# Performance work log

Hardware: AMD Instinct MI355X
Metric: run time of the kernel (lower is better)

Reference implementation:

```python
import jax, jax.numpy as jnp
import numpy as np

DIM = 1536
NHEADS = 24
HEAD_DIM = DIM // NHEADS
EPS = 1e-6


def rms_norm(x):
    # normalize over last dim, no learned weight
    ms = jnp.mean(x * x, axis=-1, keepdims=True)
    return x * jax.lax.rsqrt(ms + EPS)


def rope_non_neox(x, cos, sin):
    # x: [B, S, H, D]; cos/sin: [S, D] -> broadcast [1, S, 1, D]
    # non-neox (GPT-J / interleaved) style: pairs are (x0,x1),(x2,x3),...
    c = cos[None, :, None, :]
    s = sin[None, :, None, :]
    x1 = x[..., 0::2]
    x2 = x[..., 1::2]
    c1 = c[..., 0::2]
    s1 = s[..., 0::2]
    o1 = x1 * c1 - x2 * s1
    o2 = x2 * c1 + x1 * s1
    out = jnp.stack([o1, o2], axis=-1).reshape(x.shape)
    return out


def setup_inputs() -> dict:
    key = jax.random.key(0)
    k1, k2, k3, k4, k5 = jax.random.split(key, 5)
    B, S = 4, 4096
    x = jax.random.normal(k1, (B, S, DIM), dtype=jnp.float32)
    # rotary tables: build valid cos/sin from random angles (interleaved duplication)
    half = HEAD_DIM // 2
    inv_freq = 1.0 / (10000.0 ** (jnp.arange(0, half, dtype=jnp.float32) / half))
    t = jnp.arange(S, dtype=jnp.float32)
    freqs = jnp.outer(t, inv_freq)  # [S, D/2]
    cos = jnp.repeat(jnp.cos(freqs), 2, axis=-1)  # [S, D] interleaved
    sin = jnp.repeat(jnp.sin(freqs), 2, axis=-1)
    w_qkv = jax.random.normal(k2, (DIM, 3 * DIM), dtype=jnp.float32) * (DIM ** -0.5)
    b_qkv = jax.random.normal(k3, (3 * DIM,), dtype=jnp.float32) * 0.02
    return {"x": x, "cos": cos, "sin": sin, "w_qkv": w_qkv, "b_qkv": b_qkv}


def reference(x, cos, sin, w_qkv, b_qkv):
    B, S, _ = x.shape
    H, D = NHEADS, HEAD_DIM
    qkv = jnp.einsum('bsd,de->bse', x, w_qkv) + b_qkv  # [B,S,3*DIM]
    q, k, v = jnp.split(qkv, 3, axis=-1)
    q = q.reshape(B, S, H, D)
    k = k.reshape(B, S, H, D)
    v = v.reshape(B, S, H, D)
    q = rms_norm(q)
    k = rms_norm(k)
    q = rope_non_neox(q, cos, sin)
    k = rope_non_neox(k, cos, sin)
    # SDPA: [B,H,S,D]
    qh = q.transpose(0, 2, 1, 3)
    kh = k.transpose(0, 2, 1, 3)
    vh = v.transpose(0, 2, 1, 3)
    scale = D ** -0.5
    scores = jnp.einsum('bhqd,bhkd->bhqk', qh, kh) * scale
    attn = jax.nn.softmax(scores, axis=-1)
    out = jnp.einsum('bhqk,bhkd->bhqd', attn, vh)
    out = out.transpose(0, 2, 1, 3).reshape(B, S, H * D)
    return out
```

## Files before the change

### kernel.cpp

```cpp
#include <hip/hip_runtime.h>

#define DIM   1536
#define NQKV  4608
#define NH    24
#define HD    64
#define BATCH 4
#define SEQ   4096
#define ROWS  16384

typedef _Float16 f16x8 __attribute__((ext_vector_type(8)));
typedef float    f32x4 __attribute__((ext_vector_type(4)));

__device__ __forceinline__ void gload_lds16(const void* g, void* l) {
  __builtin_amdgcn_global_load_lds(
      (const __attribute__((address_space(1))) unsigned int*)g,
      (__attribute__((address_space(3))) unsigned int*)l, 16, 0, 0);
}
__device__ __forceinline__ float fexp2(float x) {
#if __has_builtin(__builtin_amdgcn_exp2f)
  return __builtin_amdgcn_exp2f(x);
#else
  return exp2f(x);
#endif
}

#define QSCALE 0.18033688011112042f

__global__ __launch_bounds__(256) void convert_x(const float* __restrict__ X,
                                                 _Float16* __restrict__ Xh) {
  const int i = (blockIdx.x * 256 + threadIdx.x) * 8;
  float4 a = *(const float4*)(X + i);
  float4 b = *(const float4*)(X + i + 4);
  f16x8 h;
  h[0] = (_Float16)a.x; h[1] = (_Float16)a.y; h[2] = (_Float16)a.z; h[3] = (_Float16)a.w;
  h[4] = (_Float16)b.x; h[5] = (_Float16)b.y; h[6] = (_Float16)b.z; h[7] = (_Float16)b.w;
  *(f16x8*)(Xh + i) = h;
}

__global__ __launch_bounds__(256) void transpose_w(const float* __restrict__ W,
                                                   _Float16* __restrict__ Wt) {
  __shared__ float tile[32][33];
  const int tx = threadIdx.x, ty = threadIdx.y;
  const int k0 = blockIdx.y * 32, n0 = blockIdx.x * 32;
  #pragma unroll
  for (int i = 0; i < 32; i += 8)
    tile[ty + i][tx] = W[(size_t)(k0 + ty + i) * NQKV + n0 + tx];
  __syncthreads();
  #pragma unroll
  for (int i = 0; i < 32; i += 8)
    Wt[(size_t)(n0 + ty + i) * DIM + k0 + tx] = (_Float16)tile[tx][ty + i];
}

__global__ __launch_bounds__(256) void qkv_gemm(const _Float16* __restrict__ Xh,
                                                const _Float16* __restrict__ Wt,
                                                const float* __restrict__ Bias,
                                                _Float16* __restrict__ QKV) {
  __shared__ _Float16 As[128 * 64];
  __shared__ _Float16 Bs[128 * 64];
  const int w    = threadIdx.x >> 6;
  const int lane = threadIdx.x & 63;
  const int lr   = lane >> 3, lc = lane & 7;
  const int quad = lane >> 4, l15 = lane & 15;
  const int m0 = blockIdx.y * 128;
  const int n0 = blockIdx.x * 128;
  const int waveR = (w >> 1) * 64;
  const int waveC = (w & 1) * 64;

  f32x4 acc[4][4];
  #pragma unroll
  for (int i = 0; i < 4; i++)
    #pragma unroll
    for (int j = 0; j < 4; j++) acc[i][j] = (f32x4){0.f, 0.f, 0.f, 0.f};

  for (int kt = 0; kt < DIM / 64; ++kt) {
    const int k0 = kt * 64;
    #pragma unroll
    for (int i = 0; i < 4; ++i) {
      const int rr = w * 32 + i * 8;
      gload_lds16(Xh + (size_t)(m0 + rr + lr) * DIM + k0 + lc * 8, &As[rr * 64]);
      gload_lds16(Wt + (size_t)(n0 + rr + lr) * DIM + k0 + lc * 8, &Bs[rr * 64]);
    }
    __syncthreads();
    #pragma unroll
    for (int ks = 0; ks < 2; ++ks) {
      f16x8 aF[4], bF[4];
      #pragma unroll
      for (int t = 0; t < 4; t++)
        aF[t] = *(const f16x8*)&As[(waveR + t * 16 + l15) * 64 + ks * 32 + quad * 8];
      #pragma unroll
      for (int t = 0; t < 4; t++)
        bF[t] = *(const f16x8*)&Bs[(waveC + t * 16 + l15) * 64 + ks * 32 + quad * 8];
      #pragma unroll
      for (int mt = 0; mt < 4; mt++)
        #pragma unroll
        for (int nt = 0; nt < 4; nt++)
          acc[mt][nt] = __builtin_amdgcn_mfma_f32_16x16x32_f16(aF[mt], bF[nt], acc[mt][nt], 0, 0, 0);
    }
    __syncthreads();
  }
  #pragma unroll
  for (int nt = 0; nt < 4; nt++) {
    const int n = n0 + waveC + nt * 16 + l15;
    const float bias = Bias[n];
    #pragma unroll
    for (int mt = 0; mt < 4; mt++) {
      const int mBase = m0 + waveR + mt * 16 + quad * 4;
      #pragma unroll
      for (int r = 0; r < 4; r++)
        QKV[(size_t)(mBase + r) * NQKV + n] = (_Float16)(acc[mt][nt][r] + bias);
    }
  }
}

__global__ __launch_bounds__(256) void rms_rope(_Float16* __restrict__ QKV,
                                                const float* __restrict__ Cos,
                                                const float* __restrict__ Sin) {
  const int gw   = blockIdx.x * 4 + (threadIdx.x >> 6);
  const int lane = threadIdx.x & 63;
  const int row  = gw / NH;
  const int h    = gw - row * NH;
  const int s    = row & (SEQ - 1);

  _Float16* p = QKV + (size_t)row * NQKV + h * HD;
  float q = (float)p[lane];
  float k = (float)p[DIM + lane];

  float sq = q * q, sk = k * k;
  #pragma unroll
  for (int off = 1; off < 64; off <<= 1) {
    sq += __shfl_xor(sq, off);
    sk += __shfl_xor(sk, off);
  }
  q *= rsqrtf(sq * (1.f / 64.f) + 1e-6f);
  k *= rsqrtf(sk * (1.f / 64.f) + 1e-6f);

  const float c  = Cos[s * HD + lane];
  const float si = Sin[s * HD + lane];
  const float qp = __shfl_xor(q, 1);
  const float kp = __shfl_xor(k, 1);
  float oq, ok;
  if (lane & 1) { oq = q * c + qp * si; ok = k * c + kp * si; }
  else          { oq = q * c - qp * si; ok = k * c - kp * si; }

  p[lane]       = (_Float16)(oq * QSCALE);
  p[DIM + lane] = (_Float16)ok;
}

#define LSTR 72
__global__ __launch_bounds__(256) void flash_attn(const _Float16* __restrict__ QKV,
                                                  float* __restrict__ Out) {
  __shared__ __align__(16) _Float16 sm[2 * 64 * LSTR + 4 * 32 * LSTR];
  _Float16* Ks  = sm;
  _Float16* Vts = sm + 64 * LSTR;
  const int w = threadIdx.x >> 6;
  _Float16* Ps = sm + 2 * 64 * LSTR + w * 32 * LSTR;
  const int lane = threadIdx.x & 63;
  const int quad = lane >> 4, l15 = lane & 15;
  const int bh = blockIdx.y;
  const int qt = blockIdx.x;
  const int b  = bh / NH;
  const int h  = bh - b * NH;
  const size_t rowb = (size_t)b * SEQ * NQKV + (size_t)h * HD;

  f16x8 qreg[2][2];
  #pragma unroll
  for (int mt = 0; mt < 2; mt++)
    #pragma unroll
    for (int ks = 0; ks < 2; ks++) {
      const int row = qt * 128 + w * 32 + mt * 16 + l15;
      qreg[mt][ks] = *(const f16x8*)(QKV + rowb + (size_t)row * NQKV + ks * 32 + quad * 8);
    }

  f16x8 onesF;
  {
    const _Float16 one = (_Float16)(l15 == 0 ? 1.0f : 0.0f);
    #pragma unroll
    for (int j = 0; j < 8; j++) onesF[j] = one;
  }

  f32x4 o[2][4], o4[2];
  #pragma unroll
  for (int mt = 0; mt < 2; mt++) {
    o4[mt] = (f32x4){0.f, 0.f, 0.f, 0.f};
    #pragma unroll
    for (int t = 0; t < 4; t++) o[mt][t] = (f32x4){0.f, 0.f, 0.f, 0.f};
  }

  for (int kt = 0; kt < SEQ / 64; ++kt) {
    __syncthreads();
    #pragma unroll
    for (int i = 0; i < 2; i++) {
      const int chunk = threadIdx.x + i * 256;
      const int r = chunk >> 3, c0 = (chunk & 7) * 8;
      *(uint4*)&Ks[r * LSTR + c0] =
          *(const uint4*)(QKV + rowb + (size_t)(kt * 64 + r) * NQKV + DIM + c0);
    }
    #pragma unroll
    for (int i = 0; i < 2; i++) {
      const int c0 = w * 16 + i * 8;
      union { uint4 v; _Float16 u[8]; } d;
      d.v = *(const uint4*)(QKV + rowb + (size_t)(kt * 64 + lane) * NQKV + 2 * DIM + c0);
      #pragma unroll
      for (int j = 0; j < 8; j++) Vts[(c0 + j) * LSTR + lane] = d.u[j];
    }
    __syncthreads();

    f32x4 sacc[2][4];
    #pragma unroll
    for (int mt = 0; mt < 2; mt++)
      #pragma unroll
      for (int t = 0; t < 4; t++) sacc[mt][t] = (f32x4){0.f, 0.f, 0.f, 0.f};
    #pragma unroll
    for (int ks = 0; ks < 2; ks++) {
      f16x8 bF[4];
      #pragma unroll
      for (int t = 0; t < 4; t++)
        bF[t] = *(const f16x8*)&Ks[(t * 16 + l15) * LSTR + ks * 32 + quad * 8];
      #pragma unroll
      for (int mt = 0; mt < 2; mt++)
        #pragma unroll
        for (int t = 0; t < 4; t++)
          sacc[mt][t] = __builtin_amdgcn_mfma_f32_16x16x32_f16(qreg[mt][ks], bF[t], sacc[mt][t], 0, 0, 0);
    }

    #pragma unroll
    for (int mt = 0; mt < 2; mt++)
      #pragma unroll
      for (int t = 0; t < 4; t++)
        #pragma unroll
        for (int r = 0; r < 4; r++) {
          const _Float16 ph = (_Float16)fexp2(sacc[mt][t][r]);
          Ps[(mt * 16 + quad * 4 + r) * LSTR + t * 16 + l15] = ph;
        }

    #pragma unroll
    for (int ks = 0; ks < 2; ks++) {
      f16x8 pF[2];
      #pragma unroll
      for (int mt = 0; mt < 2; mt++)
        pF[mt] = *(const f16x8*)&Ps[(mt * 16 + l15) * LSTR + ks * 32 + quad * 8];
      #pragma unroll
      for (int t = 0; t < 4; t++) {
        f16x8 vF = *(const f16x8*)&Vts[(t * 16 + l15) * LSTR + ks * 32 + quad * 8];
        #pragma unroll
        for (int mt = 0; mt < 2; mt++)
          o[mt][t] = __builtin_amdgcn_mfma_f32_16x16x32_f16(pF[mt], vF, o[mt][t], 0, 0, 0);
      }
      #pragma unroll
      for (int mt = 0; mt < 2; mt++)
        o4[mt] = __builtin_amdgcn_mfma_f32_16x16x32_f16(pF[mt], onesF, o4[mt], 0, 0, 0);
    }
  }

  #pragma unroll
  for (int mt = 0; mt < 2; mt++) {
    float lrow[4];
    #pragma unroll
    for (int r = 0; r < 4; r++) lrow[r] = __shfl(o4[mt][r], lane & 48);
    #pragma unroll
    for (int t = 0; t < 4; t++)
      #pragma unroll
      for (int r = 0; r < 4; r++) {
        const int srow = qt * 128 + w * 32 + mt * 16 + quad * 4 + r;
        const int d = t * 16 + l15;
        Out[((size_t)(b * SEQ + srow)) * DIM + h * HD + d] = o[mt][t][r] / lrow[r];
      }
  }
}

extern "C" void kernel_launch(void* const* d_in, const int* in_sizes, int n_in,
                              void* d_out, int out_size, void* d_ws, size_t ws_size,
                              hipStream_t stream) {
  const float* X    = (const float*)d_in[0];
  const float* Cos  = (const float*)d_in[1];
  const float* Sin  = (const float*)d_in[2];
  const float* W    = (const float*)d_in[3];
  const float* Bias = (const float*)d_in[4];
  float* Out = (float*)d_out;

  char* ws = (char*)d_ws;
  _Float16* Xh  = (_Float16*)(ws);
  _Float16* Wt  = (_Float16*)(ws + 50331648);
  _Float16* QKV = (_Float16*)(ws + 64487424);

  convert_x  <<<dim3(ROWS * DIM / (8 * 256)), 256, 0, stream>>>(X, Xh);
  transpose_w<<<dim3(NQKV / 32, DIM / 32), dim3(32, 8), 0, stream>>>(W, Wt);
  qkv_gemm   <<<dim3(NQKV / 128, ROWS / 128), 256, 0, stream>>>(Xh, Wt, Bias, QKV);
  rms_rope   <<<dim3(ROWS * NH / 4), 256, 0, stream>>>(QKV, Cos, Sin);
  flash_attn <<<dim3(SEQ / 128, BATCH * NH), 256, 0, stream>>>(QKV, Out);
}
```

Measured before the change: 1.276 ms.

## Double flash-attention query tile and prefetch next K/V tile into registers

Each block now handles 256 query rows, with 64 rows per wave instead of 32. Every K/V tile staged in LDS is therefore reused across twice as many queries, which halves the number of blocks and the total K/V traffic. The K and V loads for the next tile are issued into registers before the current tile's MFMA work and written to LDS after a barrier, so global load latency overlaps with compute. The cost is higher register pressure from the larger accumulators and prefetch buffers, twice the LDS for P, and fewer blocks to spread across the CUs.

```diff
diff --git a/kernel.cpp b/kernel.cpp
--- a/kernel.cpp
+++ b/kernel.cpp
@@ -149,11 +149,11 @@
 #define LSTR 72
 __global__ __launch_bounds__(256) void flash_attn(const _Float16* __restrict__ QKV,
                                                   float* __restrict__ Out) {
-  __shared__ __align__(16) _Float16 sm[2 * 64 * LSTR + 4 * 32 * LSTR];
+  __shared__ __align__(16) _Float16 sm[2 * 64 * LSTR + 4 * 64 * LSTR];
   _Float16* Ks  = sm;
   _Float16* Vts = sm + 64 * LSTR;
   const int w = threadIdx.x >> 6;
-  _Float16* Ps = sm + 2 * 64 * LSTR + w * 32 * LSTR;
+  _Float16* Ps = sm + 2 * 64 * LSTR + w * 64 * LSTR;
   const int lane = threadIdx.x & 63;
   const int quad = lane >> 4, l15 = lane & 15;
   const int bh = blockIdx.y;
@@ -162,12 +162,12 @@
   const int h  = bh - b * NH;
   const size_t rowb = (size_t)b * SEQ * NQKV + (size_t)h * HD;
 
-  f16x8 qreg[2][2];
-  #pragma unroll
-  for (int mt = 0; mt < 2; mt++)
+  f16x8 qreg[4][2];
+  #pragma unroll
+  for (int mt = 0; mt < 4; mt++)
     #pragma unroll
     for (int ks = 0; ks < 2; ks++) {
-      const int row = qt * 128 + w * 32 + mt * 16 + l15;
+      const int row = qt * 256 + w * 64 + mt * 16 + l15;
       qreg[mt][ks] = *(const f16x8*)(QKV + rowb + (size_t)row * NQKV + ks * 32 + quad * 8);
     }
 
@@ -178,36 +178,48 @@
     for (int j = 0; j < 8; j++) onesF[j] = one;
   }
 
-  f32x4 o[2][4], o4[2];
-  #pragma unroll
-  for (int mt = 0; mt < 2; mt++) {
+  f32x4 o[4][4], o4[4];
+  #pragma unroll
+  for (int mt = 0; mt < 4; mt++) {
     o4[mt] = (f32x4){0.f, 0.f, 0.f, 0.f};
     #pragma unroll
     for (int t = 0; t < 4; t++) o[mt][t] = (f32x4){0.f, 0.f, 0.f, 0.f};
+  }
+
+  const int kr  = threadIdx.x >> 3;
+  const int kc0 = (threadIdx.x & 7) * 8;
+  const int vc0base = w * 16;
+
+  #pragma unroll
+  for (int i = 0; i < 2; i++) {
+    const int r = kr + i * 32;
+    *(uint4*)&Ks[r * LSTR + kc0] =
+        *(const uint4*)(QKV + rowb + (size_t)r * NQKV + DIM + kc0);
+  }
+  #pragma unroll
+  for (int i = 0; i < 2; i++) {
+    const int c0 = vc0base + i * 8;
+    union { uint4 v; _Float16 u[8]; } d;
+    d.v = *(const uint4*)(QKV + rowb + (size_t)lane * NQKV + 2 * DIM + c0);
+    #pragma unroll
+    for (int j = 0; j < 8; j++) Vts[(c0 + j) * LSTR + lane] = d.u[j];
   }
 
   for (int kt = 0; kt < SEQ / 64; ++kt) {
     __syncthreads();
-    #pragma unroll
-    for (int i = 0; i < 2; i++) {
-      const int chunk = threadIdx.x + i * 256;
-      const int r = chunk >> 3, c0 = (chunk & 7) * 8;
-      *(uint4*)&Ks[r * LSTR + c0] =
-          *(const uint4*)(QKV + rowb + (size_t)(kt * 64 + r) * NQKV + DIM + c0);
-    }
-    #pragma unroll
-    for (int i = 0; i < 2; i++) {
-      const int c0 = w * 16 + i * 8;
-      union { uint4 v; _Float16 u[8]; } d;
-      d.v = *(const uint4*)(QKV + rowb + (size_t)(kt * 64 + lane) * NQKV + 2 * DIM + c0);
-      #pragma unroll
-      for (int j = 0; j < 8; j++) Vts[(c0 + j) * LSTR + lane] = d.u[j];
-    }
-    __syncthreads();
-
-    f32x4 sacc[2][4];
-    #pragma unroll
-    for (int mt = 0; mt < 2; mt++)
+
+    const int ktn = (kt + 1 < SEQ / 64) ? kt + 1 : kt;
+    uint4 kpre[2], vpre[2];
+    #pragma unroll
+    for (int i = 0; i < 2; i++)
+      kpre[i] = *(const uint4*)(QKV + rowb + (size_t)(ktn * 64 + kr + i * 32) * NQKV + DIM + kc0);
+    #pragma unroll
+    for (int i = 0; i < 2; i++)
+      vpre[i] = *(const uint4*)(QKV + rowb + (size_t)(ktn * 64 + lane) * NQKV + 2 * DIM + vc0base + i * 8);
+
+    f32x4 sacc[4][4];
+    #pragma unroll
+    for (int mt = 0; mt < 4; mt++)
       #pragma unroll
       for (int t = 0; t < 4; t++) sacc[mt][t] = (f32x4){0.f, 0.f, 0.f, 0.f};
     #pragma unroll
@@ -217,14 +229,14 @@
       for (int t = 0; t < 4; t++)
         bF[t] = *(const f16x8*)&Ks[(t * 16 + l15) * LSTR + ks * 32 + quad * 8];
       #pragma unroll
-      for (int mt = 0; mt < 2; mt++)
+      for (int mt = 0; mt < 4; mt++)
         #pragma unroll
         for (int t = 0; t < 4; t++)
           sacc[mt][t] = __builtin_amdgcn_mfma_f32_16x16x32_f16(qreg[mt][ks], bF[t], sacc[mt][t], 0, 0, 0);
     }
 
     #pragma unroll
-    for (int mt = 0; mt < 2; mt++)
+    for (int mt = 0; mt < 4; mt++)
       #pragma unroll
       for (int t = 0; t < 4; t++)
         #pragma unroll
@@ -235,25 +247,39 @@
 
     #pragma unroll
     for (int ks = 0; ks < 2; ks++) {
-      f16x8 pF[2];
-      #pragma unroll
-      for (int mt = 0; mt < 2; mt++)
+      f16x8 pF[4];
+      #pragma unroll
+      for (int mt = 0; mt < 4; mt++)
         pF[mt] = *(const f16x8*)&Ps[(mt * 16 + l15) * LSTR + ks * 32 + quad * 8];
       #pragma unroll
       for (int t = 0; t < 4; t++) {
         f16x8 vF = *(const f16x8*)&Vts[(t * 16 + l15) * LSTR + ks * 32 + quad * 8];
         #pragma unroll
-        for (int mt = 0; mt < 2; mt++)
+        for (int mt = 0; mt < 4; mt++)
           o[mt][t] = __builtin_amdgcn_mfma_f32_16x16x32_f16(pF[mt], vF, o[mt][t], 0, 0, 0);
       }
       #pragma unroll
-      for (int mt = 0; mt < 2; mt++)
+      for (int mt = 0; mt < 4; mt++)
         o4[mt] = __builtin_amdgcn_mfma_f32_16x16x32_f16(pF[mt], onesF, o4[mt], 0, 0, 0);
     }
-  }
-
-  #pragma unroll
-  for (int mt = 0; mt < 2; mt++) {
+
+    __syncthreads();
+
+    #pragma unroll
+    for (int i = 0; i < 2; i++)
+      *(uint4*)&Ks[(kr + i * 32) * LSTR + kc0] = kpre[i];
+    #pragma unroll
+    for (int i = 0; i < 2; i++) {
+      const int c0 = vc0base + i * 8;
+      union { uint4 v; _Float16 u[8]; } d;
+      d.v = vpre[i];
+      #pragma unroll
+      for (int j = 0; j < 8; j++) Vts[(c0 + j) * LSTR + lane] = d.u[j];
+    }
+  }
+
+  #pragma unroll
+  for (int mt = 0; mt < 4; mt++) {
     float lrow[4];
     #pragma unroll
     for (int r = 0; r < 4; r++) lrow[r] = __shfl(o4[mt][r], lane & 48);
@@ -261,7 +287,7 @@
     for (int t = 0; t < 4; t++)
       #pragma unroll
       for (int r = 0; r < 4; r++) {
-        const int srow = qt * 128 + w * 32 + mt * 16 + quad * 4 + r;
+        const int srow = qt * 256 + w * 64 + mt * 16 + quad * 4 + r;
         const int d = t * 16 + l15;
         Out[((size_t)(b * SEQ + srow)) * DIM + h * HD + d] = o[mt][t][r] / lrow[r];
       }
@@ -287,5 +313,5 @@
   transpose_w<<<dim3(NQKV / 32, DIM / 32), dim3(32, 8), 0, stream>>>(W, Wt);
   qkv_gemm   <<<dim3(NQKV / 128, ROWS / 128), 256, 0, stream>>>(Xh, Wt, Bias, QKV);
   rms_rope   <<<dim3(ROWS * NH / 4), 256, 0, stream>>>(QKV, Cos, Sin);
-  flash_attn <<<dim3(SEQ / 128, BATCH * NH), 256, 0, stream>>>(QKV, Out);
-}
+  flash_attn <<<dim3(SEQ / 256, BATCH * NH), 256, 0, stream>>>(QKV, Out);
+}
```

Result: slower. 1.471 ms (+15.3%).
